# Kernel tuning notes

Measured on AMD Instinct MI355X. Metric: run time of the kernel, lower is better.

Reference implementation:

```python
import jax, jax.numpy as jnp
import numpy as np

IN_DIM = 128
HID = 256
OUT_DIM = 10
N_NODES = 20000
N_EDGES = 320000
N_GRAPHS = 64


def setup_inputs() -> dict:
    key = jax.random.key(0)
    ks = jax.random.split(key, 20)
    x = jax.random.normal(ks[0], (N_NODES, IN_DIM), dtype=jnp.float32)
    edge_index = jax.random.randint(ks[1], (2, N_EDGES), 0, N_NODES, dtype=jnp.int64)
    batch = jnp.sort(jax.random.randint(ks[2], (N_NODES,), 0, N_GRAPHS, dtype=jnp.int64))

    def lin(k, fin, fout):
        s = 1.0 / np.sqrt(fin)
        kw, kb = jax.random.split(k)
        w = jax.random.uniform(kw, (fin, fout), jnp.float32, -s, s)
        b = jax.random.uniform(kb, (fout,), jnp.float32, -s, s)
        return w, b

    w1a, b1a = lin(ks[3], IN_DIM, HID)
    w1b, b1b = lin(ks[4], HID, HID)
    w2a, b2a = lin(ks[5], HID, HID)
    w2b, b2b = lin(ks[6], HID, HID)
    w3a, b3a = lin(ks[7], HID, HID)
    w3b, b3b = lin(ks[8], HID, HID)
    wl, bl = lin(ks[9], HID, OUT_DIM)
    return {"x": x, "edge_index": edge_index, "batch": batch,
            "w1a": w1a, "b1a": b1a, "w1b": w1b, "b1b": b1b,
            "w2a": w2a, "b2a": b2a, "w2b": w2b, "b2b": b2b,
            "w3a": w3a, "b3a": b3a, "w3b": w3b, "b3b": b3b,
            "wl": wl, "bl": bl}


def _gin_conv(x, src, dst, wa, ba, wb, bb):
    # PyG GINConv, eps=0: h_i = MLP(x_i + sum_{j->i} x_j)
    agg = jax.ops.segment_sum(x[src], dst, num_segments=N_NODES)
    h = x + agg
    h = jax.nn.relu(h @ wa + ba)
    h = jax.nn.relu(h @ wb + bb)
    return h


def reference(x, edge_index, batch,
              w1a, b1a, w1b, b1b,
              w2a, b2a, w2b, b2b,
              w3a, b3a, w3b, b3b,
              wl, bl):
    src, dst = edge_index[0], edge_index[1]
    h = _gin_conv(x, src, dst, w1a, b1a, w1b, b1b)   # extra F.relu is a no-op after ReLU MLP
    h = _gin_conv(h, src, dst, w2a, b2a, w2b, b2b)
    h = _gin_conv(h, src, dst, w3a, b3a, w3b, b3b)
    pooled = jax.ops.segment_sum(h, batch, num_segments=N_GRAPHS)  # [G, HID]
    logits = pooled @ wl + bl
    return jax.nn.log_softmax(logits, axis=1)
```

## Files before the change

kernel.cpp:

```cpp
#include <hip/hip_runtime.h>
#include <hip/hip_bf16.h>

#define N_NODES 20000
#define M_PAD 20096
#define IN_DIM 128
#define HID 256
#define OUT_DIM 10
#define N_EDGES 320000
#define N_GRAPHS 64
#define CAP 64

typedef __attribute__((ext_vector_type(8))) short bf16x8;
typedef __attribute__((ext_vector_type(8))) unsigned short u16x8;
typedef __attribute__((ext_vector_type(4))) float f32x4;
typedef __attribute__((ext_vector_type(2))) float f32x2;

__device__ inline float bf2f(unsigned short u) {
    return __uint_as_float((unsigned int)u << 16);
}
__device__ inline unsigned short f2bf(float f) {
    __hip_bfloat16 h = __float2bfloat16(f);
    return *reinterpret_cast<unsigned short*>(&h);
}

__device__ __forceinline__ void gl16(const void* g, void* l) {
    __builtin_amdgcn_global_load_lds(
        (const __attribute__((address_space(1))) unsigned int*)g,
        (__attribute__((address_space(3))) unsigned int*)l, 16, 0, 0);
}

__global__ void zero_int(int* __restrict__ p, int n) {
    int i = blockIdx.x * blockDim.x + threadIdx.x;
    if (i < n) p[i] = 0;
}

__global__ __launch_bounds__(256) void transpose_all(
    const float* __restrict__ w1a, const float* __restrict__ w1b,
    const float* __restrict__ w2a, const float* __restrict__ w2b,
    const float* __restrict__ w3a, const float* __restrict__ w3b,
    __hip_bfloat16* __restrict__ o1a, __hip_bfloat16* __restrict__ o1b,
    __hip_bfloat16* __restrict__ o2a, __hip_bfloat16* __restrict__ o2b,
    __hip_bfloat16* __restrict__ o3a, __hip_bfloat16* __restrict__ o3b,
    const float* __restrict__ x, unsigned char* __restrict__ x_f8, int n4,
    const int* __restrict__ src, const int* __restrict__ dst,
    int* __restrict__ deg, int* __restrict__ col)
{
    __shared__ float tile[32][33];
    int z = blockIdx.z;
    if (z == 6) {
        int i = (blockIdx.y * 8 + blockIdx.x) * 256 + threadIdx.x;
        for (; i < n4; i += 64 * 256) {
            float4 v = reinterpret_cast<const float4*>(x)[i];
            int w = __builtin_amdgcn_cvt_pk_fp8_f32(v.x, v.y, 0, false);
            w = __builtin_amdgcn_cvt_pk_fp8_f32(v.z, v.w, w, true);
            reinterpret_cast<unsigned int*>(x_f8)[i] = (unsigned int)w;
        }
        return;
    }
    if (z == 7) {
        int i = (blockIdx.y * 8 + blockIdx.x) * 256 + threadIdx.x;
        for (; i < N_EDGES; i += 64 * 256) {
            int d = dst[i];
            int slot = atomicAdd(&deg[d], 1);
            if (slot < CAP) col[(size_t)d * CAP + slot] = src[i];
        }
        return;
    }
    const float* in = (z == 0) ? w1a : (z == 1) ? w1b : (z == 2) ? w2a
                    : (z == 3) ? w2b : (z == 4) ? w3a : w3b;
    __hip_bfloat16* out = (z == 0) ? o1a : (z == 1) ? o1b : (z == 2) ? o2a
                        : (z == 3) ? o2b : (z == 4) ? o3a : o3b;
    int rows = (z == 0) ? IN_DIM : HID;
    int r0 = blockIdx.y * 32;
    if (r0 >= rows) return;
    int c0 = blockIdx.x * 32;
    int tx = threadIdx.x & 31, ty = threadIdx.x >> 5;
    for (int i = ty; i < 32; i += 8)
        tile[i][tx] = in[(size_t)(r0 + i) * HID + c0 + tx];
    __syncthreads();
    for (int i = ty; i < 32; i += 8)
        out[(size_t)(c0 + i) * rows + r0 + tx] = __float2bfloat16(tile[tx][i]);
}

template<int D>
__global__ __launch_bounds__(256) void gin_agg_f8(
    const unsigned char* __restrict__ X8, const int* __restrict__ deg,
    const int* __restrict__ col, __hip_bfloat16* __restrict__ out)
{
    constexpr int LPR = D / 8;
    constexpr int NPW = 64 / LPR;
    int lane = threadIdx.x & 63;
    int sub = lane / LPR;
    int lr = lane & (LPR - 1);
    int node = blockIdx.x * 4 * NPW + (threadIdx.x >> 6) * NPW + sub;
    if (node >= N_NODES) return;
    int boff = lr * 8;

    float a[8];
    {
        unsigned long long w = *reinterpret_cast<const unsigned long long*>(
            X8 + (size_t)node * D + boff);
        unsigned int lo = (unsigned int)w, hi = (unsigned int)(w >> 32);
        f32x2 p;
        p = __builtin_amdgcn_cvt_pk_f32_fp8(lo, false); a[0] = p.x; a[1] = p.y;
        p = __builtin_amdgcn_cvt_pk_f32_fp8(lo, true);  a[2] = p.x; a[3] = p.y;
        p = __builtin_amdgcn_cvt_pk_f32_fp8(hi, false); a[4] = p.x; a[5] = p.y;
        p = __builtin_amdgcn_cvt_pk_f32_fp8(hi, true);  a[6] = p.x; a[7] = p.y;
    }
    int e = deg[node];
    if (e > CAP) e = CAP;
    const int* cp = col + (size_t)node * CAP;
    int k = 0;
    for (; k + 16 <= e; k += 16) {
        unsigned long long w[16];
        #pragma unroll
        for (int j = 0; j < 16; ++j)
            w[j] = *reinterpret_cast<const unsigned long long*>(
                X8 + (size_t)cp[k + j] * D + boff);
        #pragma unroll
        for (int j = 0; j < 16; ++j) {
            unsigned int lo = (unsigned int)w[j], hi = (unsigned int)(w[j] >> 32);
            f32x2 p;
            p = __builtin_amdgcn_cvt_pk_f32_fp8(lo, false); a[0] += p.x; a[1] += p.y;
            p = __builtin_amdgcn_cvt_pk_f32_fp8(lo, true);  a[2] += p.x; a[3] += p.y;
            p = __builtin_amdgcn_cvt_pk_f32_fp8(hi, false); a[4] += p.x; a[5] += p.y;
            p = __builtin_amdgcn_cvt_pk_f32_fp8(hi, true);  a[6] += p.x; a[7] += p.y;
        }
    }
    if (k + 8 <= e) {
        unsigned long long w[8];
        #pragma unroll
        for (int j = 0; j < 8; ++j)
            w[j] = *reinterpret_cast<const unsigned long long*>(
                X8 + (size_t)cp[k + j] * D + boff);
        #pragma unroll
        for (int j = 0; j < 8; ++j) {
            unsigned int lo = (unsigned int)w[j], hi = (unsigned int)(w[j] >> 32);
            f32x2 p;
            p = __builtin_amdgcn_cvt_pk_f32_fp8(lo, false); a[0] += p.x; a[1] += p.y;
            p = __builtin_amdgcn_cvt_pk_f32_fp8(lo, true);  a[2] += p.x; a[3] += p.y;
            p = __builtin_amdgcn_cvt_pk_f32_fp8(hi, false); a[4] += p.x; a[5] += p.y;
            p = __builtin_amdgcn_cvt_pk_f32_fp8(hi, true);  a[6] += p.x; a[7] += p.y;
        }
        k += 8;
    }
    for (; k < e; ++k) {
        unsigned long long w = *reinterpret_cast<const unsigned long long*>(
            X8 + (size_t)cp[k] * D + boff);
        unsigned int lo = (unsigned int)w, hi = (unsigned int)(w >> 32);
        f32x2 p;
        p = __builtin_amdgcn_cvt_pk_f32_fp8(lo, false); a[0] += p.x; a[1] += p.y;
        p = __builtin_amdgcn_cvt_pk_f32_fp8(lo, true);  a[2] += p.x; a[3] += p.y;
        p = __builtin_amdgcn_cvt_pk_f32_fp8(hi, false); a[4] += p.x; a[5] += p.y;
        p = __builtin_amdgcn_cvt_pk_f32_fp8(hi, true);  a[6] += p.x; a[7] += p.y;
    }
    u16x8 o;
    #pragma unroll
    for (int p8 = 0; p8 < 8; ++p8) o[p8] = f2bf(a[p8]);
    *reinterpret_cast<u16x8*>((unsigned short*)out + (size_t)node * D + lr * 8) = o;
}

template<int K1, int MODE>
__global__ __launch_bounds__(256) void gin_mlp(
    const __hip_bfloat16* __restrict__ A, const __hip_bfloat16* __restrict__ W1t,
    const float* __restrict__ b1, const __hip_bfloat16* __restrict__ W2t,
    const float* __restrict__ b2, __hip_bfloat16* __restrict__ C,
    unsigned char* __restrict__ C8,
    const int* __restrict__ batch, float* __restrict__ pooled)
{
    __shared__ int4 smem4[4672];
    char* smem = (char*)smem4;
    char* mid = smem + 40960;
    int* sbatch = (int*)(smem + 73728);

    int tid = threadIdx.x;
    int lane = tid & 63;
    int wid = tid >> 6;
    int m0 = blockIdx.x * 64;

    int r16 = lane & 15;
    int g = lane >> 4;
    int gg = g ^ ((r16 >> 1) & 3);

    int rseg = lane >> 2;
    int sw = (lane & 3) ^ ((lane >> 3) & 3);
    int rA = wid * 16 + rseg;

    const char* gA = (const char*)A + (size_t)(m0 + rA) * (K1 * 2) + sw * 16;
    const char* gW1[4];
    #pragma unroll
    for (int j = 0; j < 4; ++j) {
        int rW = (wid + 4 * j) * 16 + rseg;
        gW1[j] = (const char*)W1t + (size_t)rW * (K1 * 2) + sw * 16;
    }

    auto stage1 = [&](int buf, int t) {
        char* l = smem + buf * 20480;
        gl16(gA + t * 64, l + wid * 1024);
        #pragma unroll
        for (int j = 0; j < 4; ++j)
            gl16(gW1[j] + t * 64, l + 4096 + (wid + 4 * j) * 1024);
    };

    f32x4 acc[4][4] = {};
    constexpr int NT1 = K1 / 32;

    stage1(0, 0);
    __syncthreads();
    #pragma unroll
    for (int t = 0; t < NT1; ++t) {
        int cur = t & 1;
        if (t + 1 < NT1) stage1(cur ^ 1, t + 1);
        const char* As = smem + cur * 20480;
        const char* Bs = As + 4096;
        bf16x8 af[4], bfv[4];
        #pragma unroll
        for (int m = 0; m < 4; ++m)
            af[m] = *reinterpret_cast<const bf16x8*>(As + (m * 16 + r16) * 64 + gg * 16);
        #pragma unroll
        for (int n = 0; n < 4; ++n)
            bfv[n] = *reinterpret_cast<const bf16x8*>(Bs + (wid * 64 + n * 16 + r16) * 64 + gg * 16);
        #pragma unroll
        for (int m = 0; m < 4; ++m)
            #pragma unroll
            for (int n = 0; n < 4; ++n)
                acc[m][n] = __builtin_amdgcn_mfma_f32_16x16x32_bf16(af[m], bfv[n], acc[m][n], 0, 0, 0);
        __syncthreads();
    }

    const char* gW2[4];
    #pragma unroll
    for (int j = 0; j < 4; ++j) {
        int rW = (wid + 4 * j) * 16 + rseg;
        gW2[j] = (const char*)W2t + (size_t)rW * 512 + sw * 16;
    }
    auto stageW2 = [&](int buf, int t) {
        char* l = smem + buf * 16384;
        #pragma unroll
        for (int j = 0; j < 4; ++j)
            gl16(gW2[j] + t * 64, l + (wid + 4 * j) * 1024);
    };
    stageW2(0, 0);

    #pragma unroll
    for (int m = 0; m < 4; ++m) {
        #pragma unroll
        for (int n = 0; n < 4; ++n) {
            int colX = wid * 64 + n * 16 + r16;
            float bb = b1[colX];
            int cb = colX >> 3;
            int within = (colX & 7) * 2;
            #pragma unroll
            for (int r = 0; r < 4; ++r) {
                int row = m * 16 + g * 4 + r;
                float v = fmaxf(acc[m][n][r] + bb, 0.f);
                *reinterpret_cast<unsigned short*>(
                    mid + row * 512 + ((cb ^ (row & 7)) << 4) + within) = f2bf(v);
            }
        }
    }

    __syncthreads();

    f32x4 acc2[4][4] = {};
    #pragma unroll
    for (int t = 0; t < 8; ++t) {
        int cur = t & 1;
        if (t + 1 < 8) stageW2(cur ^ 1, t + 1);
        const char* Bs = smem + cur * 16384;
        bf16x8 af[4], bfv[4];
        #pragma unroll
        for (int m = 0; m < 4; ++m) {
            int row = m * 16 + r16;
            int c = (t * 4 + g) ^ (row & 7);
            af[m] = *reinterpret_cast<const bf16x8*>(mid + row * 512 + c * 16);
        }
        #pragma unroll
        for (int n = 0; n < 4; ++n)
            bfv[n] = *reinterpret_cast<const bf16x8*>(Bs + (wid * 64 + n * 16 + r16) * 64 + gg * 16);
        #pragma unroll
        for (int m = 0; m < 4; ++m)
            #pragma unroll
            for (int n = 0; n < 4; ++n)
                acc2[m][n] = __builtin_amdgcn_mfma_f32_16x16x32_bf16(af[m], bfv[n], acc2[m][n], 0, 0, 0);
        __syncthreads();
    }

    if constexpr (MODE == 2) {
        #pragma unroll
        for (int m = 0; m < 4; ++m) {
            #pragma unroll
            for (int n = 0; n < 4; ++n) {
                int colX = wid * 64 + n * 16 + r16;
                float bb = b2[colX];
                #pragma unroll
                for (int r = 0; r < 4; ++r) {
                    int row = m * 16 + g * 4 + r;
                    float v = fmaxf(acc2[m][n][r] + bb, 0.f);
                    *reinterpret_cast<unsigned short*>(mid + row * 512 + colX * 2) = f2bf(v);
                }
            }
        }
        int rlim = N_NODES - m0;
        if (rlim > 64) rlim = 64;
        if (tid < 64 && tid < rlim) sbatch[tid] = batch[m0 + tid];
        __syncthreads();
        if (rlim > 0) {
            int colp = tid;
            float pacc = 0.f;
            int cur = sbatch[0];
            for (int i = 0; i < rlim; ++i) {
                int gph = sbatch[i];
                if (gph != cur) { atomicAdd(&pooled[cur * HID + colp], pacc); pacc = 0.f; cur = gph; }
                pacc += bf2f(*reinterpret_cast<unsigned short*>(mid + i * 512 + colp * 2));
            }
            atomicAdd(&pooled[cur * HID + colp], pacc);
        }
    } else {
        #pragma unroll
        for (int m = 0; m < 4; ++m) {
            #pragma unroll
            for (int n = 0; n < 4; ++n) {
                int colX = wid * 64 + n * 16 + r16;
                float bb = b2[colX];
                #pragma unroll
                for (int r = 0; r < 4; ++r) {
                    int row = m0 + m * 16 + g * 4 + r;
                    float v = fmaxf(acc2[m][n][r] + bb, 0.f);
                    if constexpr (MODE == 1) {
                        int b = __builtin_amdgcn_cvt_pk_fp8_f32(v, 0.f, 0, false);
                        C8[(size_t)row * HID + colX] = (unsigned char)(b & 0xff);
                    } else {
                        C[(size_t)row * HID + colX] = __float2bfloat16(v);
                    }
                }
            }
        }
    }
}

__global__ __launch_bounds__(256) void head_kernel(
    const float* __restrict__ pooled, const float* __restrict__ wl,
    const float* __restrict__ bl, float* __restrict__ out)
{
    int gph = blockIdx.x;
    int d = threadIdx.x;
    __shared__ float p[HID];
    __shared__ float logits[OUT_DIM];
    __shared__ float lse_s;
    p[d] = pooled[gph * HID + d];
    __syncthreads();
    if (d < OUT_DIM) {
        float v = bl[d];
        for (int k = 0; k < HID; ++k) v += p[k] * wl[k * OUT_DIM + d];
        logits[d] = v;
    }
    __syncthreads();
    if (d == 0) {
        float mx = logits[0];
        for (int j = 1; j < OUT_DIM; ++j) mx = fmaxf(mx, logits[j]);
        float s = 0.f;
        for (int j = 0; j < OUT_DIM; ++j) s += expf(logits[j] - mx);
        lse_s = mx + logf(s);
    }
    __syncthreads();
    if (d < OUT_DIM) out[gph * OUT_DIM + d] = logits[d] - lse_s;
}

extern "C" void kernel_launch(void* const* d_in, const int* in_sizes, int n_in,
                              void* d_out, int out_size, void* d_ws, size_t ws_size,
                              hipStream_t stream) {
    const float* x    = (const float*)d_in[0];
    const int*   ei   = (const int*)d_in[1];
    const int*   batch= (const int*)d_in[2];
    const float* w1a  = (const float*)d_in[3];
    const float* b1a  = (const float*)d_in[4];
    const float* w1b  = (const float*)d_in[5];
    const float* b1b  = (const float*)d_in[6];
    const float* w2a  = (const float*)d_in[7];
    const float* b2a  = (const float*)d_in[8];
    const float* w2b  = (const float*)d_in[9];
    const float* b2b  = (const float*)d_in[10];
    const float* w3a  = (const float*)d_in[11];
    const float* b3a  = (const float*)d_in[12];
    const float* w3b  = (const float*)d_in[13];
    const float* b3b  = (const float*)d_in[14];
    const float* wl   = (const float*)d_in[15];
    const float* bl   = (const float*)d_in[16];

    const int* src = ei;
    const int* dst = ei + N_EDGES;

    __hip_bfloat16* bufA = (__hip_bfloat16*)d_ws;
    __hip_bfloat16* bufB = bufA + (size_t)M_PAD * HID;
    unsigned char*  h8   = (unsigned char*)(bufB + (size_t)M_PAD * HID);
    unsigned char*  x_f8 = h8 + (size_t)M_PAD * HID;
    __hip_bfloat16* wt1a = (__hip_bfloat16*)(x_f8 + (size_t)N_NODES * IN_DIM);
    __hip_bfloat16* wt1b = wt1a + HID * IN_DIM;
    __hip_bfloat16* wt2a = wt1b + HID * HID;
    __hip_bfloat16* wt2b = wt2a + HID * HID;
    __hip_bfloat16* wt3a = wt2b + HID * HID;
    __hip_bfloat16* wt3b = wt3a + HID * HID;
    float* pooled = (float*)(wt3b + HID * HID);
    int* deg     = (int*)(pooled + N_GRAPHS * HID);
    int* col     = deg + N_NODES;

    float* out = (float*)d_out;

    int zn = N_GRAPHS * HID + N_NODES;
    zero_int<<<(zn + 255) / 256, 256, 0, stream>>>((int*)pooled, zn);

    int n4 = N_NODES * IN_DIM / 4;
    transpose_all<<<dim3(8, 8, 8), 256, 0, stream>>>(
        w1a, w1b, w2a, w2b, w3a, w3b, wt1a, wt1b, wt2a, wt2b, wt3a, wt3b,
        x, x_f8, n4, src, dst, deg, col);

    int agg128_blocks = (N_NODES + 15) / 16;
    int agg256_blocks = (N_NODES + 7) / 8;
    int mlp_blocks = M_PAD / 64;

    gin_agg_f8<IN_DIM><<<agg128_blocks, 256, 0, stream>>>(x_f8, deg, col, bufA);
    gin_mlp<IN_DIM, 1><<<mlp_blocks, 256, 0, stream>>>(bufA, wt1a, b1a, wt1b, b1b, bufB, h8, batch, pooled);

    gin_agg_f8<HID><<<agg256_blocks, 256, 0, stream>>>(h8, deg, col, bufA);
    gin_mlp<HID, 1><<<mlp_blocks, 256, 0, stream>>>(bufA, wt2a, b2a, wt2b, b2b, bufB, h8, batch, pooled);

    gin_agg_f8<HID><<<agg256_blocks, 256, 0, stream>>>(h8, deg, col, bufA);
    gin_mlp<HID, 2><<<mlp_blocks, 256, 0, stream>>>(bufA, wt3a, b3a, wt3b, b3b, bufB, h8, batch, pooled);

    head_kernel<<<N_GRAPHS, 256, 0, stream>>>(pooled, wl, bl, out);
}
```

Before: 141.3 us.

## Fuse GIN layers and head into persistent megakernel with grid barriers

```diff
diff --git a/kernel.cpp b/kernel.cpp
--- a/kernel.cpp
+++ b/kernel.cpp
@@ -9,6 +9,8 @@
 #define N_EDGES 320000
 #define N_GRAPHS 64
 #define CAP 64
+#define MLP_BLOCKS (M_PAD / 64)
+#define MEGA_GRID 512
 
 typedef __attribute__((ext_vector_type(8))) short bf16x8;
 typedef __attribute__((ext_vector_type(8))) unsigned short u16x8;
@@ -27,6 +29,18 @@
     __builtin_amdgcn_global_load_lds(
         (const __attribute__((address_space(1))) unsigned int*)g,
         (__attribute__((address_space(3))) unsigned int*)l, 16, 0, 0);
+}
+
+__device__ __forceinline__ void gbar(int* ctr) {
+    __syncthreads();
+    if (threadIdx.x == 0) {
+        __threadfence();
+        atomicAdd(ctr, 1);
+        while (atomicAdd(ctr, 0) < MEGA_GRID)
+            __builtin_amdgcn_s_sleep(8);
+        __threadfence();
+    }
+    __syncthreads();
 }
 
 __global__ void zero_int(int* __restrict__ p, int n) {
@@ -83,7 +97,7 @@
 }
 
 template<int D>
-__global__ __launch_bounds__(256) void gin_agg_f8(
+__device__ void gather_phase(
     const unsigned char* __restrict__ X8, const int* __restrict__ deg,
     const int* __restrict__ col, __hip_bfloat16* __restrict__ out)
 {
@@ -92,84 +106,83 @@
     int lane = threadIdx.x & 63;
     int sub = lane / LPR;
     int lr = lane & (LPR - 1);
-    int node = blockIdx.x * 4 * NPW + (threadIdx.x >> 6) * NPW + sub;
-    if (node >= N_NODES) return;
     int boff = lr * 8;
-
-    float a[8];
-    {
-        unsigned long long w = *reinterpret_cast<const unsigned long long*>(
-            X8 + (size_t)node * D + boff);
-        unsigned int lo = (unsigned int)w, hi = (unsigned int)(w >> 32);
-        f32x2 p;
-        p = __builtin_amdgcn_cvt_pk_f32_fp8(lo, false); a[0] = p.x; a[1] = p.y;
-        p = __builtin_amdgcn_cvt_pk_f32_fp8(lo, true);  a[2] = p.x; a[3] = p.y;
-        p = __builtin_amdgcn_cvt_pk_f32_fp8(hi, false); a[4] = p.x; a[5] = p.y;
-        p = __builtin_amdgcn_cvt_pk_f32_fp8(hi, true);  a[6] = p.x; a[7] = p.y;
-    }
-    int e = deg[node];
-    if (e > CAP) e = CAP;
-    const int* cp = col + (size_t)node * CAP;
-    int k = 0;
-    for (; k + 16 <= e; k += 16) {
-        unsigned long long w[16];
-        #pragma unroll
-        for (int j = 0; j < 16; ++j)
-            w[j] = *reinterpret_cast<const unsigned long long*>(
-                X8 + (size_t)cp[k + j] * D + boff);
-        #pragma unroll
-        for (int j = 0; j < 16; ++j) {
-            unsigned int lo = (unsigned int)w[j], hi = (unsigned int)(w[j] >> 32);
+    int wslot = blockIdx.x * 4 + (threadIdx.x >> 6);
+    int stride = MEGA_GRID * 4 * NPW;
+
+    for (int node = wslot * NPW + sub; node < N_NODES; node += stride) {
+        float a[8];
+        {
+            unsigned long long w = *reinterpret_cast<const unsigned long long*>(
+                X8 + (size_t)node * D + boff);
+            unsigned int lo = (unsigned int)w, hi = (unsigned int)(w >> 32);
+            f32x2 p;
+            p = __builtin_amdgcn_cvt_pk_f32_fp8(lo, false); a[0] = p.x; a[1] = p.y;
+            p = __builtin_amdgcn_cvt_pk_f32_fp8(lo, true);  a[2] = p.x; a[3] = p.y;
+            p = __builtin_amdgcn_cvt_pk_f32_fp8(hi, false); a[4] = p.x; a[5] = p.y;
+            p = __builtin_amdgcn_cvt_pk_f32_fp8(hi, true);  a[6] = p.x; a[7] = p.y;
+        }
+        int e = deg[node];
+        if (e > CAP) e = CAP;
+        const int* cp = col + (size_t)node * CAP;
+        int k = 0;
+        for (; k + 16 <= e; k += 16) {
+            unsigned long long w[16];
+            #pragma unroll
+            for (int j = 0; j < 16; ++j)
+                w[j] = *reinterpret_cast<const unsigned long long*>(
+                    X8 + (size_t)cp[k + j] * D + boff);
+            #pragma unroll
+            for (int j = 0; j < 16; ++j) {
+                unsigned int lo = (unsigned int)w[j], hi = (unsigned int)(w[j] >> 32);
+                f32x2 p;
+                p = __builtin_amdgcn_cvt_pk_f32_fp8(lo, false); a[0] += p.x; a[1] += p.y;
+                p = __builtin_amdgcn_cvt_pk_f32_fp8(lo, true);  a[2] += p.x; a[3] += p.y;
+                p = __builtin_amdgcn_cvt_pk_f32_fp8(hi, false); a[4] += p.x; a[5] += p.y;
+                p = __builtin_amdgcn_cvt_pk_f32_fp8(hi, true);  a[6] += p.x; a[7] += p.y;
+            }
+        }
+        if (k + 8 <= e) {
+            unsigned long long w[8];
+            #pragma unroll
+            for (int j = 0; j < 8; ++j)
+                w[j] = *reinterpret_cast<const unsigned long long*>(
+                    X8 + (size_t)cp[k + j] * D + boff);
+            #pragma unroll
+            for (int j = 0; j < 8; ++j) {
+                unsigned int lo = (unsigned int)w[j], hi = (unsigned int)(w[j] >> 32);
+                f32x2 p;
+                p = __builtin_amdgcn_cvt_pk_f32_fp8(lo, false); a[0] += p.x; a[1] += p.y;
+                p = __builtin_amdgcn_cvt_pk_f32_fp8(lo, true);  a[2] += p.x; a[3] += p.y;
+                p = __builtin_amdgcn_cvt_pk_f32_fp8(hi, false); a[4] += p.x; a[5] += p.y;
+                p = __builtin_amdgcn_cvt_pk_f32_fp8(hi, true);  a[6] += p.x; a[7] += p.y;
+            }
+            k += 8;
+        }
+        for (; k < e; ++k) {
+            unsigned long long w = *reinterpret_cast<const unsigned long long*>(
+                X8 + (size_t)cp[k] * D + boff);
+            unsigned int lo = (unsigned int)w, hi = (unsigned int)(w >> 32);
             f32x2 p;
             p = __builtin_amdgcn_cvt_pk_f32_fp8(lo, false); a[0] += p.x; a[1] += p.y;
             p = __builtin_amdgcn_cvt_pk_f32_fp8(lo, true);  a[2] += p.x; a[3] += p.y;
             p = __builtin_amdgcn_cvt_pk_f32_fp8(hi, false); a[4] += p.x; a[5] += p.y;
             p = __builtin_amdgcn_cvt_pk_f32_fp8(hi, true);  a[6] += p.x; a[7] += p.y;
         }
-    }
-    if (k + 8 <= e) {
-        unsigned long long w[8];
-        #pragma unroll
-        for (int j = 0; j < 8; ++j)
-            w[j] = *reinterpret_cast<const unsigned long long*>(
-                X8 + (size_t)cp[k + j] * D + boff);
-        #pragma unroll
-        for (int j = 0; j < 8; ++j) {
-            unsigned int lo = (unsigned int)w[j], hi = (unsigned int)(w[j] >> 32);
-            f32x2 p;
-            p = __builtin_amdgcn_cvt_pk_f32_fp8(lo, false); a[0] += p.x; a[1] += p.y;
-            p = __builtin_amdgcn_cvt_pk_f32_fp8(lo, true);  a[2] += p.x; a[3] += p.y;
-            p = __builtin_amdgcn_cvt_pk_f32_fp8(hi, false); a[4] += p.x; a[5] += p.y;
-            p = __builtin_amdgcn_cvt_pk_f32_fp8(hi, true);  a[6] += p.x; a[7] += p.y;
-        }
-        k += 8;
-    }
-    for (; k < e; ++k) {
-        unsigned long long w = *reinterpret_cast<const unsigned long long*>(
-            X8 + (size_t)cp[k] * D + boff);
-        unsigned int lo = (unsigned int)w, hi = (unsigned int)(w >> 32);
-        f32x2 p;
-        p = __builtin_amdgcn_cvt_pk_f32_fp8(lo, false); a[0] += p.x; a[1] += p.y;
-        p = __builtin_amdgcn_cvt_pk_f32_fp8(lo, true);  a[2] += p.x; a[3] += p.y;
-        p = __builtin_amdgcn_cvt_pk_f32_fp8(hi, false); a[4] += p.x; a[5] += p.y;
-        p = __builtin_amdgcn_cvt_pk_f32_fp8(hi, true);  a[6] += p.x; a[7] += p.y;
-    }
-    u16x8 o;
-    #pragma unroll
-    for (int p8 = 0; p8 < 8; ++p8) o[p8] = f2bf(a[p8]);
-    *reinterpret_cast<u16x8*>((unsigned short*)out + (size_t)node * D + lr * 8) = o;
+        u16x8 o;
+        #pragma unroll
+        for (int p8 = 0; p8 < 8; ++p8) o[p8] = f2bf(a[p8]);
+        *reinterpret_cast<u16x8*>((unsigned short*)out + (size_t)node * D + lr * 8) = o;
+    }
 }
 
 template<int K1, int MODE>
-__global__ __launch_bounds__(256) void gin_mlp(
+__device__ void mlp_phase(
     const __hip_bfloat16* __restrict__ A, const __hip_bfloat16* __restrict__ W1t,
     const float* __restrict__ b1, const __hip_bfloat16* __restrict__ W2t,
-    const float* __restrict__ b2, __hip_bfloat16* __restrict__ C,
-    unsigned char* __restrict__ C8,
-    const int* __restrict__ batch, float* __restrict__ pooled)
+    const float* __restrict__ b2, unsigned char* __restrict__ C8,
+    const int* __restrict__ batch, float* __restrict__ pooled, char* smem)
 {
-    __shared__ int4 smem4[4672];
-    char* smem = (char*)smem4;
     char* mid = smem + 40960;
     int* sbatch = (int*)(smem + 73728);
 
@@ -327,27 +340,23 @@
                 for (int r = 0; r < 4; ++r) {
                     int row = m0 + m * 16 + g * 4 + r;
                     float v = fmaxf(acc2[m][n][r] + bb, 0.f);
-                    if constexpr (MODE == 1) {
-                        int b = __builtin_amdgcn_cvt_pk_fp8_f32(v, 0.f, 0, false);
-                        C8[(size_t)row * HID + colX] = (unsigned char)(b & 0xff);
-                    } else {
-                        C[(size_t)row * HID + colX] = __float2bfloat16(v);
-                    }
+                    int b = __builtin_amdgcn_cvt_pk_fp8_f32(v, 0.f, 0, false);
+                    C8[(size_t)row * HID + colX] = (unsigned char)(b & 0xff);
                 }
             }
         }
     }
 }
 
-__global__ __launch_bounds__(256) void head_kernel(
+__device__ void head_phase(
     const float* __restrict__ pooled, const float* __restrict__ wl,
-    const float* __restrict__ bl, float* __restrict__ out)
+    const float* __restrict__ bl, float* __restrict__ out, char* smem)
 {
     int gph = blockIdx.x;
     int d = threadIdx.x;
-    __shared__ float p[HID];
-    __shared__ float logits[OUT_DIM];
-    __shared__ float lse_s;
+    float* p = (float*)smem;
+    float* logits = p + HID;
+    float* lse_s = logits + OUT_DIM;
     p[d] = pooled[gph * HID + d];
     __syncthreads();
     if (d < OUT_DIM) {
@@ -361,10 +370,47 @@
         for (int j = 1; j < OUT_DIM; ++j) mx = fmaxf(mx, logits[j]);
         float s = 0.f;
         for (int j = 0; j < OUT_DIM; ++j) s += expf(logits[j] - mx);
-        lse_s = mx + logf(s);
-    }
-    __syncthreads();
-    if (d < OUT_DIM) out[gph * OUT_DIM + d] = logits[d] - lse_s;
+        *lse_s = mx + logf(s);
+    }
+    __syncthreads();
+    if (d < OUT_DIM) out[gph * OUT_DIM + d] = logits[d] - *lse_s;
+}
+
+__global__ __launch_bounds__(256, 2) void gin_mega(
+    const unsigned char* x_f8, const int* deg, const int* col, const int* batch,
+    const __hip_bfloat16* wt1a, const float* b1a,
+    const __hip_bfloat16* wt1b, const float* b1b,
+    const __hip_bfloat16* wt2a, const float* b2a,
+    const __hip_bfloat16* wt2b, const float* b2b,
+    const __hip_bfloat16* wt3a, const float* b3a,
+    const __hip_bfloat16* wt3b, const float* b3b,
+    const float* wl, const float* bl,
+    __hip_bfloat16* bufA, unsigned char* h8,
+    float* pooled, float* out, int* bars)
+{
+    __shared__ int4 smem4[4672];
+    char* smem = (char*)smem4;
+
+    gather_phase<IN_DIM>(x_f8, deg, col, bufA);
+    gbar(&bars[0]);
+    if (blockIdx.x < MLP_BLOCKS)
+        mlp_phase<IN_DIM, 1>(bufA, wt1a, b1a, wt1b, b1b, h8, batch, pooled, smem);
+    gbar(&bars[1]);
+
+    gather_phase<HID>(h8, deg, col, bufA);
+    gbar(&bars[2]);
+    if (blockIdx.x < MLP_BLOCKS)
+        mlp_phase<HID, 1>(bufA, wt2a, b2a, wt2b, b2b, h8, batch, pooled, smem);
+    gbar(&bars[3]);
+
+    gather_phase<HID>(h8, deg, col, bufA);
+    gbar(&bars[4]);
+    if (blockIdx.x < MLP_BLOCKS)
+        mlp_phase<HID, 2>(bufA, wt3a, b3a, wt3b, b3b, h8, batch, pooled, smem);
+    gbar(&bars[5]);
+
+    if (blockIdx.x < N_GRAPHS)
+        head_phase(pooled, wl, bl, out, smem);
 }
 
 extern "C" void kernel_launch(void* const* d_in, const int* in_sizes, int n_in,
@@ -403,11 +449,12 @@
     __hip_bfloat16* wt3b = wt3a + HID * HID;
     float* pooled = (float*)(wt3b + HID * HID);
     int* deg     = (int*)(pooled + N_GRAPHS * HID);
-    int* col     = deg + N_NODES;
+    int* bars    = deg + N_NODES;
+    int* col     = bars + 8;
 
     float* out = (float*)d_out;
 
-    int zn = N_GRAPHS * HID + N_NODES;
+    int zn = N_GRAPHS * HID + N_NODES + 8;
     zero_int<<<(zn + 255) / 256, 256, 0, stream>>>((int*)pooled, zn);
 
     int n4 = N_NODES * IN_DIM / 4;
@@ -415,18 +462,8 @@
         w1a, w1b, w2a, w2b, w3a, w3b, wt1a, wt1b, wt2a, wt2b, wt3a, wt3b,
         x, x_f8, n4, src, dst, deg, col);
 
-    int agg128_blocks = (N_NODES + 15) / 16;
-    int agg256_blocks = (N_NODES + 7) / 8;
-    int mlp_blocks = M_PAD / 64;
-
-    gin_agg_f8<IN_DIM><<<agg128_blocks, 256, 0, stream>>>(x_f8, deg, col, bufA);
-    gin_mlp<IN_DIM, 1><<<mlp_blocks, 256, 0, stream>>>(bufA, wt1a, b1a, wt1b, b1b, bufB, h8, batch, pooled);
-
-    gin_agg_f8<HID><<<agg256_blocks, 256, 0, stream>>>(h8, deg, col, bufA);
-    gin_mlp<HID, 1><<<mlp_blocks, 256, 0, stream>>>(bufA, wt2a, b2a, wt2b, b2b, bufB, h8, batch, pooled);
-
-    gin_agg_f8<HID><<<agg256_blocks, 256, 0, stream>>>(h8, deg, col, bufA);
-    gin_mlp<HID, 2><<<mlp_blocks, 256, 0, stream>>>(bufA, wt3a, b3a, wt3b, b3b, bufB, h8, batch, pooled);
-
-    head_kernel<<<N_GRAPHS, 256, 0, stream>>>(pooled, wl, bl, out);
-}
+    gin_mega<<<MEGA_GRID, 256, 0, stream>>>(
+        x_f8, deg, col, batch,
+        wt1a, b1a, wt1b, b1b, wt2a, b2a, wt2b, b2b, wt3a, b3a, wt3b, b3b,
+        wl, bl, bufA, h8, pooled, out, bars);
+}
```

Measured after the change: 451.0 us. 3.19x slower.
